# Optimization experiments

Measured on AMD Instinct MI355X. Metric: run time of the kernel, lower is better.

## Reference

```python
import jax, jax.numpy as jnp
import numpy as np
import math

IN_DIM = 3
N_LEVELS = 16
F = 2
LOG2_T = 19
T = 2 ** LOG2_T
BASE_RES = 16
FINEST_RES = 512
N_POINTS = 1048576

# Per-level resolutions (static, matches torch buffer construction)
_b = math.exp((math.log(FINEST_RES) - math.log(BASE_RES)) / max(N_LEVELS - 1, 1))
RES = np.array([int(BASE_RES * _b ** i) for i in range(N_LEVELS)], dtype=np.int32)  # [L]
# XOR spatial-hash primes (dim 0 uses prime 1)
PRIMES = np.array([1, 2654435761, 805459861, 3674653429], dtype=np.uint32)


def _hash(coords_u32):
    """coords_u32: (..., IN_DIM) uint32 -> int32 hash in [0, T).
    uint32 wraparound arithmetic gives the same low-19 bits as torch's int64
    math, since T divides 2**32 and XOR/product low bits are self-contained."""
    h = coords_u32[..., 0]
    for d in range(1, IN_DIM):
        h = h ^ (coords_u32[..., d] * PRIMES[d % len(PRIMES)])
    return (h & jnp.uint32(T - 1)).astype(jnp.int32)


def setup_inputs() -> dict:
    key = jax.random.key(0)
    k1, k2 = jax.random.split(key)
    x = jax.random.uniform(k1, (N_POINTS, IN_DIM), dtype=jnp.float32)  # coords in [0,1]
    embeddings = jax.random.uniform(
        k2, (N_LEVELS, T, F), minval=-1e-4, maxval=1e-4, dtype=jnp.float32
    )
    return {"x": x, "embeddings": embeddings}


def reference(x, embeddings):
    N = x.shape[0]
    res_f = jnp.asarray(RES, dtype=x.dtype)            # [L]
    res_i = jnp.asarray(RES, dtype=jnp.int32)          # [L]

    # Scale all levels at once: [L, N, D]
    x_scaled = x[None, :, :] * (res_f[:, None, None] - 1.0)
    x_floor = jnp.clip(x_scaled.astype(jnp.int32), 0, res_i[:, None, None] - 2)
    x_frac = x_scaled - x_floor.astype(x.dtype)        # [L, N, D]

    feat = jnp.zeros((N_LEVELS, N, F), dtype=x.dtype)
    for corner in range(2 ** IN_DIM):                  # fixed 8 corners
        off = np.array([(corner >> d) & 1 for d in range(IN_DIM)], dtype=np.int32)
        corner_coords = jnp.clip(x_floor + off, 0, res_i[:, None, None] - 1)
        h = _hash(corner_coords.astype(jnp.uint32))    # [L, N]
        # gather per-level features: embeddings[l, h[l, n]] -> [L, N, F]
        corner_feat = jnp.take_along_axis(embeddings, h[:, :, None], axis=1)
        # N-linear weight: prod over dims of frac or (1-frac)
        w = jnp.prod(
            jnp.where(off.astype(bool), x_frac, 1.0 - x_frac),
            axis=-1, keepdims=True,
        )                                              # [L, N, 1]
        feat = feat + w * corner_feat

    # concat levels along feature dim: [N, L*F]
    return jnp.moveaxis(feat, 0, 1).reshape(N, N_LEVELS * F)
```

## Files before the change

### kernel.cpp

```cpp
#include <hip/hip_runtime.h>
#include <math.h>
#include <stdint.h>

#define LOG2_T 19
#define T_SIZE (1u << LOG2_T)
#define T_MASK (T_SIZE - 1u)
#define N_LEVELS 16
#define N_DENSE 8
#define PRIME1 2654435761u
#define PRIME2 805459861u

typedef unsigned long long u64;
typedef float f4v __attribute__((ext_vector_type(4)));

struct Params {
    int res[N_LEVELS];
    int brick[N_DENSE];
    int off[N_DENSE];
    int dense_total;
};

__device__ __forceinline__ float bf_lo(uint32_t v) { return __uint_as_float(v << 16); }
__device__ __forceinline__ float bf_hi(uint32_t v) { return __uint_as_float(v & 0xFFFF0000u); }

__device__ __forceinline__ uint32_t f32_to_bf16_rne(float f) {
    uint32_t u = __float_as_uint(f);
    u += 0x7FFFu + ((u >> 16) & 1u);
    return u >> 16;
}
__device__ __forceinline__ uint32_t pack2(float2 e) {
    return f32_to_bf16_rne(e.x) | (f32_to_bf16_rne(e.y) << 16);
}

__device__ __forceinline__ void nt_store_f2(float2 v, float2* p) {
    union { float2 f; u64 u; } cv; cv.f = v;
    __builtin_nontemporal_store(cv.u, (u64*)p);
}
__device__ __forceinline__ float2 nt_load_f2(const float2* p) {
    union { float2 f; u64 u; } cv;
    cv.u = __builtin_nontemporal_load((const u64*)p);
    return cv.f;
}

__device__ __forceinline__ void pair_load(const uint32_t* __restrict__ t,
                                          uint32_t h0, uint32_t& e0, uint32_t& e1) {
    const uint2 q = *(const uint2*)(t + (h0 & ~1u));
    const bool hi = (h0 & 1u);
    e0 = hi ? q.y : q.x;
    e1 = hi ? q.x : q.y;
}

__global__ __launch_bounds__(256) void hg_build_fine(
    const float2* __restrict__ emb, uint32_t* __restrict__ tabF)
{
    const int i = blockIdx.x * 256 + threadIdx.x;
    tabF[i] = pack2(emb[(size_t)N_DENSE * T_SIZE + i]);
}

__global__ __launch_bounds__(256) void hg_build_dense(
    const float2* __restrict__ emb, uint32_t* __restrict__ tabD, Params P)
{
    const int i = blockIdx.x * 256 + threadIdx.x;
    if (i >= P.dense_total) return;
    int l = 0;
    while (l < N_DENSE - 1 && i >= P.off[l + 1]) ++l;
    const int e = i - P.off[l];
    const int B = P.brick[l], R = P.res[l];
    const int sub = e & 7, br = e >> 3;
    int bx = br % B; int t2 = br / B; int by = t2 % B; int bz = t2 / B;
    int x = bx * 2 + (sub & 1);        if (x > R - 1) x = R - 1;
    int y = by * 2 + ((sub >> 1) & 1); if (y > R - 1) y = R - 1;
    int z = bz * 2 + (sub >> 2);       if (z > R - 1) z = R - 1;
    const uint32_t h = ((uint32_t)x ^ ((uint32_t)y * PRIME1) ^ ((uint32_t)z * PRIME2)) & T_MASK;
    tabD[i] = pack2(emb[(size_t)l * T_SIZE + h]);
}

struct Pt { int ix, iy, iz; float fx, fy, fz; };

__device__ __forceinline__ Pt prep_point(const float* __restrict__ x, int n,
                                         int rl, float rf) {
    Pt p;
    const float sx = x[n * 3 + 0] * rf;
    const float sy = x[n * 3 + 1] * rf;
    const float sz = x[n * 3 + 2] * rf;
    int ix = (int)sx; ix = ix < 0 ? 0 : (ix > rl - 2 ? rl - 2 : ix);
    int iy = (int)sy; iy = iy < 0 ? 0 : (iy > rl - 2 ? rl - 2 : iy);
    int iz = (int)sz; iz = iz < 0 ? 0 : (iz > rl - 2 ? rl - 2 : iz);
    p.ix = ix; p.iy = iy; p.iz = iz;
    p.fx = sx - (float)ix; p.fy = sy - (float)iy; p.fz = sz - (float)iz;
    return p;
}

__device__ __forceinline__ void gather_fine(const uint32_t* __restrict__ t,
                                            const Pt& p, uint32_t c[8]) {
    const uint32_t hx0 = (uint32_t)p.ix;
    const uint32_t hy0 = (uint32_t)p.iy * PRIME1, hy1 = hy0 + PRIME1;
    const uint32_t hz0 = (uint32_t)p.iz * PRIME2, hz1 = hz0 + PRIME2;
    const uint32_t n00 = hy0 ^ hz0, n10 = hy1 ^ hz0, n01 = hy0 ^ hz1, n11 = hy1 ^ hz1;
    if ((p.ix & 1) == 0) {
        pair_load(t, (hx0 ^ n00) & T_MASK, c[0], c[1]);
        pair_load(t, (hx0 ^ n10) & T_MASK, c[2], c[3]);
        pair_load(t, (hx0 ^ n01) & T_MASK, c[4], c[5]);
        pair_load(t, (hx0 ^ n11) & T_MASK, c[6], c[7]);
    } else {
        const uint32_t hx1 = hx0 + 1u;
        c[0] = t[(hx0 ^ n00) & T_MASK]; c[1] = t[(hx1 ^ n00) & T_MASK];
        c[2] = t[(hx0 ^ n10) & T_MASK]; c[3] = t[(hx1 ^ n10) & T_MASK];
        c[4] = t[(hx0 ^ n01) & T_MASK]; c[5] = t[(hx1 ^ n01) & T_MASK];
        c[6] = t[(hx0 ^ n11) & T_MASK]; c[7] = t[(hx1 ^ n11) & T_MASK];
    }
}

__device__ __forceinline__ void gather_dense(const uint32_t* __restrict__ t,
                                             int B, const Pt& p, uint32_t c[8]) {
    const int ix = p.ix, iy = p.iy, iz = p.iz;
    const int bx0 = ix >> 1, sx0 = ix & 1;
    const int by0 = iy >> 1, sy0 = iy & 1, by1 = (iy + 1) >> 1, sy1 = (iy + 1) & 1;
    const int bz0 = iz >> 1, sz0 = iz & 1, bz1 = (iz + 1) >> 1, sz1 = (iz + 1) & 1;
    const int zy00 = (((bz0 * B + by0) * B) << 3) | (sy0 << 1) | (sz0 << 2);
    const int zy10 = (((bz0 * B + by1) * B) << 3) | (sy1 << 1) | (sz0 << 2);
    const int zy01 = (((bz1 * B + by0) * B) << 3) | (sy0 << 1) | (sz1 << 2);
    const int zy11 = (((bz1 * B + by1) * B) << 3) | (sy1 << 1) | (sz1 << 2);
    if (sx0 == 0) {
        if (sy0 == 0) {
            const uint4 q0 = *(const uint4*)(t + zy00 + (bx0 << 3));
            const uint4 q1 = *(const uint4*)(t + zy01 + (bx0 << 3));
            c[0] = q0.x; c[1] = q0.y; c[2] = q0.z; c[3] = q0.w;
            c[4] = q1.x; c[5] = q1.y; c[6] = q1.z; c[7] = q1.w;
        } else {
            const uint2 q0 = *(const uint2*)(t + zy00 + (bx0 << 3));
            const uint2 q1 = *(const uint2*)(t + zy10 + (bx0 << 3));
            const uint2 q2 = *(const uint2*)(t + zy01 + (bx0 << 3));
            const uint2 q3 = *(const uint2*)(t + zy11 + (bx0 << 3));
            c[0] = q0.x; c[1] = q0.y; c[2] = q1.x; c[3] = q1.y;
            c[4] = q2.x; c[5] = q2.y; c[6] = q3.x; c[7] = q3.y;
        }
    } else {
        const int bx1 = bx0 + 1;
        c[0] = t[zy00 + (bx0 << 3) + 1]; c[1] = t[zy00 + (bx1 << 3)];
        c[2] = t[zy10 + (bx0 << 3) + 1]; c[3] = t[zy10 + (bx1 << 3)];
        c[4] = t[zy01 + (bx0 << 3) + 1]; c[5] = t[zy01 + (bx1 << 3)];
        c[6] = t[zy11 + (bx0 << 3) + 1]; c[7] = t[zy11 + (bx1 << 3)];
    }
}

__device__ __forceinline__ float2 blend8(const uint32_t c[8], const Pt& p) {
    const float wx0 = 1.0f - p.fx, wx1 = p.fx;
    const float wy0 = 1.0f - p.fy, wy1 = p.fy;
    const float wz0 = 1.0f - p.fz, wz1 = p.fz;
    float w, f0 = 0.0f, f1 = 0.0f;
    w = wx0 * wy0 * wz0; f0 = fmaf(w, bf_lo(c[0]), f0); f1 = fmaf(w, bf_hi(c[0]), f1);
    w = wx1 * wy0 * wz0; f0 = fmaf(w, bf_lo(c[1]), f0); f1 = fmaf(w, bf_hi(c[1]), f1);
    w = wx0 * wy1 * wz0; f0 = fmaf(w, bf_lo(c[2]), f0); f1 = fmaf(w, bf_hi(c[2]), f1);
    w = wx1 * wy1 * wz0; f0 = fmaf(w, bf_lo(c[3]), f0); f1 = fmaf(w, bf_hi(c[3]), f1);
    w = wx0 * wy0 * wz1; f0 = fmaf(w, bf_lo(c[4]), f0); f1 = fmaf(w, bf_hi(c[4]), f1);
    w = wx1 * wy0 * wz1; f0 = fmaf(w, bf_lo(c[5]), f0); f1 = fmaf(w, bf_hi(c[5]), f1);
    w = wx0 * wy1 * wz1; f0 = fmaf(w, bf_lo(c[6]), f0); f1 = fmaf(w, bf_hi(c[6]), f1);
    w = wx1 * wy1 * wz1; f0 = fmaf(w, bf_lo(c[7]), f0); f1 = fmaf(w, bf_hi(c[7]), f1);
    float2 o; o.x = f0; o.y = f1;
    return o;
}

__global__ __launch_bounds__(256) void hg_levels(
    const float* __restrict__ x,
    const uint32_t* __restrict__ tabF,
    const uint32_t* __restrict__ tabD,
    float2* __restrict__ feat,
    int N, Params P)
{
    const int l  = blockIdx.x & 15;
    const int n0 = (blockIdx.x >> 4) * 512 + threadIdx.x;
    if (n0 >= N) return;
    const int n1 = n0 + 256;
    const bool hasB = (n1 < N);
    const int nB = hasB ? n1 : n0;

    const int   rl = P.res[l];
    const float rf = (float)(rl - 1);

    const Pt pA = prep_point(x, n0, rl, rf);
    const Pt pB = prep_point(x, nB, rl, rf);

    uint32_t cA[8], cB[8];
    if (l >= N_DENSE) {
        const uint32_t* __restrict__ t = tabF + (size_t)(l - N_DENSE) * T_SIZE;
        gather_fine(t, pA, cA);
        gather_fine(t, pB, cB);
    } else {
        const uint32_t* __restrict__ t = tabD + P.off[l];
        const int B = P.brick[l];
        gather_dense(t, B, pA, cA);
        gather_dense(t, B, pB, cB);
    }

    nt_store_f2(blend8(cA, pA), &feat[(size_t)l * N + n0]);
    if (hasB)
        nt_store_f2(blend8(cB, pB), &feat[(size_t)l * N + n1]);
}

__global__ __launch_bounds__(256) void hg_transpose(
    const float2* __restrict__ feat, f4v* __restrict__ out, int N)
{
    __shared__ float2 st[N_LEVELS][33];
    const int base = blockIdx.x * 32;
    const int t = threadIdx.x;
#pragma unroll
    for (int i = 0; i < 2; ++i) {
        const int idx = i * 256 + t;
        const int l = idx >> 5, p = idx & 31;
        const int n = base + p;
        st[l][p] = (n < N) ? nt_load_f2(&feat[(size_t)l * N + n]) : make_float2(0.f, 0.f);
    }
    __syncthreads();
    const int p = t >> 3, k = t & 7;
    const int n = base + p;
    if (n < N) {
        const float2 a = st[2 * k][p], b = st[2 * k + 1][p];
        f4v o; o.x = a.x; o.y = a.y; o.z = b.x; o.w = b.y;
        __builtin_nontemporal_store(o, &out[(size_t)n * 8 + k]);
    }
}

__global__ __launch_bounds__(256) void hg_fallback(
    const float* __restrict__ x, const float* __restrict__ emb,
    float* __restrict__ out, int N, Params P)
{
    const int gid = blockIdx.x * 256 + threadIdx.x;
    const int n = gid >> 4, l = gid & 15;
    if (n >= N) return;
    const int rl = P.res[l];
    const float rf = (float)(rl - 1);
    float sx = x[n * 3 + 0] * rf, sy = x[n * 3 + 1] * rf, sz = x[n * 3 + 2] * rf;
    int ix = (int)sx; ix = ix < 0 ? 0 : (ix > rl - 2 ? rl - 2 : ix);
    int iy = (int)sy; iy = iy < 0 ? 0 : (iy > rl - 2 ? rl - 2 : iy);
    int iz = (int)sz; iz = iz < 0 ? 0 : (iz > rl - 2 ? rl - 2 : iz);
    const float fx = sx - ix, fy = sy - iy, fz = sz - iz;
    const uint32_t hx0 = (uint32_t)ix, hx1 = hx0 + 1u;
    const uint32_t hy0 = (uint32_t)iy * PRIME1, hy1 = hy0 + PRIME1;
    const uint32_t hz0 = (uint32_t)iz * PRIME2, hz1 = hz0 + PRIME2;
    const float2* tab = (const float2*)emb + (size_t)l * T_SIZE;
    float2 e0 = tab[(hx0 ^ hy0 ^ hz0) & T_MASK], e1 = tab[(hx1 ^ hy0 ^ hz0) & T_MASK];
    float2 e2 = tab[(hx0 ^ hy1 ^ hz0) & T_MASK], e3 = tab[(hx1 ^ hy1 ^ hz0) & T_MASK];
    float2 e4 = tab[(hx0 ^ hy0 ^ hz1) & T_MASK], e5 = tab[(hx1 ^ hy0 ^ hz1) & T_MASK];
    float2 e6 = tab[(hx0 ^ hy1 ^ hz1) & T_MASK], e7 = tab[(hx1 ^ hy1 ^ hz1) & T_MASK];
    const float wx0 = 1.0f - fx, wx1 = fx, wy0 = 1.0f - fy, wy1 = fy, wz0 = 1.0f - fz, wz1 = fz;
    float w, f0 = 0.0f, f1 = 0.0f;
    w = wx0 * wy0 * wz0; f0 = fmaf(w, e0.x, f0); f1 = fmaf(w, e0.y, f1);
    w = wx1 * wy0 * wz0; f0 = fmaf(w, e1.x, f0); f1 = fmaf(w, e1.y, f1);
    w = wx0 * wy1 * wz0; f0 = fmaf(w, e2.x, f0); f1 = fmaf(w, e2.y, f1);
    w = wx1 * wy1 * wz0; f0 = fmaf(w, e3.x, f0); f1 = fmaf(w, e3.y, f1);
    w = wx0 * wy0 * wz1; f0 = fmaf(w, e4.x, f0); f1 = fmaf(w, e4.y, f1);
    w = wx1 * wy0 * wz1; f0 = fmaf(w, e5.x, f0); f1 = fmaf(w, e5.y, f1);
    w = wx0 * wy1 * wz1; f0 = fmaf(w, e6.x, f0); f1 = fmaf(w, e6.y, f1);
    w = wx1 * wy1 * wz1; f0 = fmaf(w, e7.x, f0); f1 = fmaf(w, e7.y, f1);
    float2 o; o.x = f0; o.y = f1;
    ((float2*)out)[(size_t)n * N_LEVELS + l] = o;
}

extern "C" void kernel_launch(void* const* d_in, const int* in_sizes, int n_in,
                              void* d_out, int out_size, void* d_ws, size_t ws_size,
                              hipStream_t stream) {
    const float* x   = (const float*)d_in[0];
    const float* emb = (const float*)d_in[1];
    const int N = in_sizes[0] / 3;

    Params P;
    const double b = exp((log(512.0) - log(16.0)) / 15.0);
    for (int i = 0; i < N_LEVELS; ++i)
        P.res[i] = (int)(16.0 * pow(b, (double)i));
    int acc = 0;
    for (int i = 0; i < N_DENSE; ++i) {
        P.brick[i] = (P.res[i] + 1) >> 1;
        P.off[i] = acc;
        acc += P.brick[i] * P.brick[i] * P.brick[i] * 8;
    }
    P.dense_total = acc;

    const size_t fine_bytes  = (size_t)N_DENSE * T_SIZE * sizeof(uint32_t);
    const size_t dense_bytes = ((size_t)acc * sizeof(uint32_t) + 255) & ~255ull;
    const size_t feat_bytes  = (size_t)N_LEVELS * N * sizeof(float2);

    if (ws_size >= fine_bytes + dense_bytes + feat_bytes) {
        uint32_t* tabF = (uint32_t*)d_ws;
        uint32_t* tabD = (uint32_t*)((char*)d_ws + fine_bytes);
        float2*   feat = (float2*)((char*)d_ws + fine_bytes + dense_bytes);

        hipLaunchKernelGGL(hg_build_fine, dim3(N_DENSE * T_SIZE / 256), dim3(256), 0, stream,
                           (const float2*)emb, tabF);
        hipLaunchKernelGGL(hg_build_dense, dim3((P.dense_total + 255) / 256), dim3(256), 0, stream,
                           (const float2*)emb, tabD, P);

        const int chunks = (N + 511) / 512;
        hipLaunchKernelGGL(hg_levels, dim3(chunks * N_LEVELS), dim3(256), 0, stream,
                           x, tabF, tabD, feat, N, P);

        hipLaunchKernelGGL(hg_transpose, dim3((N + 31) / 32), dim3(256), 0, stream,
                           feat, (f4v*)d_out, N);
    } else {
        hipLaunchKernelGGL(hg_fallback, dim3((N * 16 + 255) / 256), dim3(256), 0, stream,
                           x, emb, (float*)d_out, N, P);
    }
}
```

Before: 518.3 us.

## Pair each dense level with a fine level per block to overlap gathers

Each block now handles one dense level (0-7) and one hashed fine level (8-15) for the same 512 points, instead of one level per block. The x coordinates are loaded once and reused for both levels. All 32 gathers are issued before any blending, with a sched_barrier keeping them grouped, and launch bounds request 4 blocks per CU. This is meant to balance cheap dense lookups against expensive random fine lookups inside each block, raise memory-level parallelism and halve x reloads, at the cost of higher register pressure.

```diff
diff --git a/kernel.cpp b/kernel.cpp
--- a/kernel.cpp
+++ b/kernel.cpp
@@ -77,12 +77,10 @@
 
 struct Pt { int ix, iy, iz; float fx, fy, fz; };
 
-__device__ __forceinline__ Pt prep_point(const float* __restrict__ x, int n,
-                                         int rl, float rf) {
+__device__ __forceinline__ Pt mk_pt(float x0, float x1, float x2,
+                                    int rl, float rf) {
     Pt p;
-    const float sx = x[n * 3 + 0] * rf;
-    const float sy = x[n * 3 + 1] * rf;
-    const float sz = x[n * 3 + 2] * rf;
+    const float sx = x0 * rf, sy = x1 * rf, sz = x2 * rf;
     int ix = (int)sx; ix = ix < 0 ? 0 : (ix > rl - 2 ? rl - 2 : ix);
     int iy = (int)sy; iy = iy < 0 ? 0 : (iy > rl - 2 ? rl - 2 : iy);
     int iz = (int)sz; iz = iz < 0 ? 0 : (iz > rl - 2 ? rl - 2 : iz);
@@ -161,41 +159,54 @@
     return o;
 }
 
-__global__ __launch_bounds__(256) void hg_levels(
+__global__ __launch_bounds__(256, 4) void hg_levels(
     const float* __restrict__ x,
     const uint32_t* __restrict__ tabF,
     const uint32_t* __restrict__ tabD,
     float2* __restrict__ feat,
     int N, Params P)
 {
-    const int l  = blockIdx.x & 15;
-    const int n0 = (blockIdx.x >> 4) * 512 + threadIdx.x;
+    const int l  = blockIdx.x & 7;
+    const int lf = l + 8;
+    const int n0 = (blockIdx.x >> 3) * 512 + threadIdx.x;
     if (n0 >= N) return;
     const int n1 = n0 + 256;
     const bool hasB = (n1 < N);
     const int nB = hasB ? n1 : n0;
 
-    const int   rl = P.res[l];
-    const float rf = (float)(rl - 1);
-
-    const Pt pA = prep_point(x, n0, rl, rf);
-    const Pt pB = prep_point(x, nB, rl, rf);
-
-    uint32_t cA[8], cB[8];
-    if (l >= N_DENSE) {
-        const uint32_t* __restrict__ t = tabF + (size_t)(l - N_DENSE) * T_SIZE;
-        gather_fine(t, pA, cA);
-        gather_fine(t, pB, cB);
-    } else {
-        const uint32_t* __restrict__ t = tabD + P.off[l];
-        const int B = P.brick[l];
-        gather_dense(t, B, pA, cA);
-        gather_dense(t, B, pB, cB);
-    }
-
-    nt_store_f2(blend8(cA, pA), &feat[(size_t)l * N + n0]);
-    if (hasB)
-        nt_store_f2(blend8(cB, pB), &feat[(size_t)l * N + n1]);
+    const float xa0 = x[n0 * 3 + 0], xa1 = x[n0 * 3 + 1], xa2 = x[n0 * 3 + 2];
+    const float xb0 = x[nB * 3 + 0], xb1 = x[nB * 3 + 1], xb2 = x[nB * 3 + 2];
+
+    const int   rd  = P.res[l];  const float rdf = (float)(rd - 1);
+    const int   rfi = P.res[lf]; const float rff = (float)(rfi - 1);
+
+    const Pt fA = mk_pt(xa0, xa1, xa2, rfi, rff);
+    const Pt fB = mk_pt(xb0, xb1, xb2, rfi, rff);
+    const Pt dA = mk_pt(xa0, xa1, xa2, rd, rdf);
+    const Pt dB = mk_pt(xb0, xb1, xb2, rd, rdf);
+
+    uint32_t cfA[8], cfB[8], cdA[8], cdB[8];
+    const uint32_t* __restrict__ tf = tabF + (size_t)l * T_SIZE;
+    gather_fine(tf, fA, cfA);
+    gather_fine(tf, fB, cfB);
+    const uint32_t* __restrict__ td = tabD + P.off[l];
+    const int B = P.brick[l];
+    gather_dense(td, B, dA, cdA);
+    gather_dense(td, B, dB, cdB);
+
+    __builtin_amdgcn_sched_barrier(0);
+
+    const float2 oFA = blend8(cfA, fA);
+    const float2 oFB = blend8(cfB, fB);
+    const float2 oDA = blend8(cdA, dA);
+    const float2 oDB = blend8(cdB, dB);
+
+    nt_store_f2(oDA, &feat[(size_t)l  * N + n0]);
+    nt_store_f2(oFA, &feat[(size_t)lf * N + n0]);
+    if (hasB) {
+        nt_store_f2(oDB, &feat[(size_t)l  * N + n1]);
+        nt_store_f2(oFB, &feat[(size_t)lf * N + n1]);
+    }
 }
 
 __global__ __launch_bounds__(256) void hg_transpose(
@@ -291,7 +302,7 @@
                            (const float2*)emb, tabD, P);
 
         const int chunks = (N + 511) / 512;
-        hipLaunchKernelGGL(hg_levels, dim3(chunks * N_LEVELS), dim3(256), 0, stream,
+        hipLaunchKernelGGL(hg_levels, dim3(chunks * 8), dim3(256), 0, stream,
                            x, tabF, tabD, feat, N, P);
 
         hipLaunchKernelGGL(hg_transpose, dim3((N + 31) / 32), dim3(256), 0, stream,
```

Result: no change. 519.0 us (+0.1%).
